# Kernel tuning notes

Measured on AMD Instinct MI355X. Metric: run time of the kernel, lower is better.

## Reference

```python
import jax, jax.numpy as jnp
import numpy as np

N_NODES = 32
N_EDGES = N_NODES * (N_NODES - 1)  # 992
BATCH = 16
SEQ = 8
BS = BATCH * SEQ  # 128 frames
D = 256  # node_latent_dim == edge_latent_dim
ITERS = 3


def gru_cell(x, h, Wih, Whh, bih, bhh):
    # torch GRUCell: gates ordered (r, z, n)
    gi = x @ Wih.T + bih
    gh = h @ Whh.T + bhh
    ir, iz, inn = jnp.split(gi, 3, axis=-1)
    hr, hz, hn = jnp.split(gh, 3, axis=-1)
    r = jax.nn.sigmoid(ir + hr)
    z = jax.nn.sigmoid(iz + hz)
    n = jnp.tanh(inn + r * hn)
    return (1.0 - z) * n + z * h


def setup_inputs() -> dict:
    key = jax.random.key(0)
    ks = jax.random.split(key, 16)
    s = 0.05
    inp = {
        'node_latents': jax.random.normal(ks[0], (BS * N_NODES, D), jnp.float32),
        'edge_latents': jax.random.normal(ks[1], (BS * N_EDGES, D), jnp.float32),
        'node_Wih': jax.random.normal(ks[2], (3 * D, D), jnp.float32) * s,
        'node_Whh': jax.random.normal(ks[3], (3 * D, D), jnp.float32) * s,
        'node_bih': jax.random.normal(ks[4], (3 * D,), jnp.float32) * s,
        'node_bhh': jax.random.normal(ks[5], (3 * D,), jnp.float32) * s,
        'edge_Wih': jax.random.normal(ks[6], (3 * D, D), jnp.float32) * s,
        'edge_Whh': jax.random.normal(ks[7], (3 * D, D), jnp.float32) * s,
        'edge_bih': jax.random.normal(ks[8], (3 * D,), jnp.float32) * s,
        'edge_bhh': jax.random.normal(ks[9], (3 * D,), jnp.float32) * s,
        'w_node_pool': jax.random.normal(ks[10], (2 * D,), jnp.float32) * s,
        'w_edge_pool_sub': jax.random.normal(ks[11], (2 * D,), jnp.float32) * s,
        'w_edge_pool_obj': jax.random.normal(ks[12], (2 * D,), jnp.float32) * s,
    }
    # all ordered (subject, object) pairs with subject != object, same for every frame
    pairs = np.array([(i, j) for i in range(N_NODES) for j in range(N_NODES) if i != j], dtype=np.int32)  # [E,2]
    e2n = np.concatenate([np.arange(N_EDGES, dtype=np.int32)[:, None], pairs], axis=1)  # [E,3]
    inp['edge_idx_to_node_idxs'] = jnp.asarray(np.broadcast_to(e2n, (BS, N_EDGES, 3)).copy())
    return inp


def reference(node_latents, edge_latents, node_Wih, node_Whh, node_bih, node_bhh,
              edge_Wih, edge_Whh, edge_bih, edge_bhh,
              w_node_pool, w_edge_pool_sub, w_edge_pool_obj, edge_idx_to_node_idxs):
    sub = edge_idx_to_node_idxs[..., 1].astype(jnp.int32)  # [BS,E]
    obj = edge_idx_to_node_idxs[..., 2].astype(jnp.int32)
    bidx = jnp.arange(BS, dtype=jnp.int32)[:, None]
    sub_flat = (bidx * N_NODES + sub).reshape(-1)  # [BS*E]
    obj_flat = (bidx * N_NODES + obj).reshape(-1)

    # initial GRU call with zero hidden state (torch GRUCell default)
    node_hidden = gru_cell(node_latents, jnp.zeros_like(node_latents), node_Wih, node_Whh, node_bih, node_bhh)
    edge_hidden = gru_cell(edge_latents, jnp.zeros_like(edge_latents), edge_Wih, edge_Whh, edge_bih, edge_bhh)

    for _ in range(ITERS):
        nh = node_hidden.reshape(BS, N_NODES, D)
        eh = edge_hidden.reshape(BS, N_EDGES, D)
        ns = jnp.take_along_axis(nh, sub[:, :, None], axis=1)  # [BS,E,D] subject node feats
        no = jnp.take_along_axis(nh, obj[:, :, None], axis=1)  # [BS,E,D]
        cat_s = jnp.concatenate([ns, eh], axis=-1)  # [BS,E,2D]
        cat_o = jnp.concatenate([no, eh], axis=-1)
        g_node = jax.nn.sigmoid(cat_s @ w_node_pool)[..., None]        # [BS,E,1]
        g_sub = jax.nn.sigmoid(cat_s @ w_edge_pool_sub)[..., None]
        g_obj = jax.nn.sigmoid(cat_o @ w_edge_pool_obj)[..., None]
        # node message: gated edge features scattered to subject and object nodes
        # (equivalent to the dense 0/1 incidence matmul since subject != object per edge)
        msg_e = (g_node * eh).reshape(-1, D)  # [BS*E,D]
        node_msg = (jax.ops.segment_sum(msg_e, sub_flat, num_segments=BS * N_NODES)
                    + jax.ops.segment_sum(msg_e, obj_flat, num_segments=BS * N_NODES))  # [BS*N,D]
        edge_msg = (g_sub * ns + g_obj * no).reshape(-1, D)  # [BS*E,D]
        node_hidden = gru_cell(node_msg, node_hidden, node_Wih, node_Whh, node_bih, node_bhh)
        edge_hidden = gru_cell(edge_msg, edge_hidden, edge_Wih, edge_Whh, edge_bih, edge_bhh)

    return (node_hidden.reshape(BS, N_NODES, D), edge_hidden.reshape(BS, N_EDGES, D))
```

## Files before the change

### kernel.cpp

```cpp
#include <hip/hip_runtime.h>


#define D_DIM 256
#define NNODE 32
#define NEDGE 992
#define EDGE_ROWS (128 * NEDGE)
#define NODE_ROWS (128 * NNODE)
#define BM 64
#define EGRID (EDGE_ROWS / BM)
#define NGRID (NODE_ROWS / BM)
#define GI_OFF 32768
#define GI_STR 776

typedef _Float16 half8 __attribute__((ext_vector_type(8)));
typedef _Float16 half4v __attribute__((ext_vector_type(4)));
typedef __attribute__((ext_vector_type(4))) float f32x4;

__device__ __forceinline__ float sigf(float x) { return 1.0f / (1.0f + __expf(-x)); }
__device__ __forceinline__ float tanh_fast(float x) { return 2.0f / (1.0f + __expf(-2.0f * x)) - 1.0f; }
__device__ __forceinline__ float dot4(float4 a, float4 b) { return a.x*b.x + a.y*b.y + a.z*b.z + a.w*b.w; }

__global__ __launch_bounds__(64) void pack_w(const float* __restrict__ Wih,
                                             const float* __restrict__ Whh,
                                             _Float16* __restrict__ ph) {
  const int ct = blockIdx.x;
  const int ks = blockIdx.y;
  const int l = threadIdx.x;
  const int col = ct * 16 + (l & 15);
  const int kb = ks * 32 + (l >> 4) * 8;
  const float* src = (kb < 256) ? (Wih + col * 256 + kb) : (Whh + col * 256 + (kb - 256));
  half8 v;
  #pragma unroll
  for (int j = 0; j < 8; ++j) v[j] = (_Float16)src[j];
  *(half8*)(ph + ((ct * 16 + ks) * 64 + l) * 8) = v;
}

__global__ __launch_bounds__(1024, 4) void gru_init(
    const float* __restrict__ xe, const float* __restrict__ xn,
    _Float16* __restrict__ eh16, float* __restrict__ hn,
    const _Float16* __restrict__ wpe, const _Float16* __restrict__ wpn,
    const float* __restrict__ ebih, const float* __restrict__ ebhh,
    const float* __restrict__ nbih, const float* __restrict__ nbhh) {
  __shared__ __align__(16) unsigned char lds[32768];
  const bool edge = blockIdx.x < EGRID;
  const int bx = edge ? blockIdx.x : (blockIdx.x - EGRID);
  const float* xsrc = edge ? xe : xn;
  const _Float16* wp = edge ? wpe : wpn;
  const float* bih = edge ? ebih : nbih;
  const float* bhh = edge ? ebhh : nbhh;

  const int t = threadIdx.x;
  const int rb = bx * BM;
  const int srow = t >> 4;
  const int skc = t & 15;
  const int w = t >> 6;
  const int l = t & 63;
  const int lq = l >> 4;
  const int lr = l & 15;
  const int swm = (lr & 7) << 4;
  const int swz = (srow & 7) << 4;
  const int rowg = rb + srow;

  #pragma unroll
  for (int c = 0; c < 2; ++c) {
    half8 hx;
    #pragma unroll
    for (int pq = 0; pq < 2; ++pq) {
      const float4 a = *(const float4*)(xsrc + rowg * D_DIM + c * 128 + skc * 8 + pq * 4);
      hx[pq * 4 + 0] = (_Float16)a.x; hx[pq * 4 + 1] = (_Float16)a.y;
      hx[pq * 4 + 2] = (_Float16)a.z; hx[pq * 4 + 3] = (_Float16)a.w;
    }
    *(half8*)(&lds[(srow * 512 + c * 256 + skc * 16) ^ swz]) = hx;
  }
  __syncthreads();

  const f32x4 zz = {0.f, 0.f, 0.f, 0.f};
  f32x4 acc_r[4] = {zz, zz, zz, zz};
  f32x4 acc_z[4] = {zz, zz, zz, zz};
  f32x4 acc_nx[4] = {zz, zz, zz, zz};

  #pragma unroll
  for (int ksg = 0; ksg < 8; ++ksg) {
    half8 ah[4];
    #pragma unroll
    for (int rf = 0; rf < 4; ++rf)
      ah[rf] = *(const half8*)(&lds[((rf * 16 + lr) * 512 + ksg * 64 + lq * 16) ^ swm]);
    const half8 br_ = *(const half8*)(wp + (((0 * 16 + w) * 16 + ksg) * 64 + l) * 8);
    const half8 bz_ = *(const half8*)(wp + (((1 * 16 + w) * 16 + ksg) * 64 + l) * 8);
    const half8 bn_ = *(const half8*)(wp + (((2 * 16 + w) * 16 + ksg) * 64 + l) * 8);
    #pragma unroll
    for (int rf = 0; rf < 4; ++rf)
      acc_r[rf] = __builtin_amdgcn_mfma_f32_16x16x32_f16(ah[rf], br_, acc_r[rf], 0, 0, 0);
    #pragma unroll
    for (int rf = 0; rf < 4; ++rf)
      acc_z[rf] = __builtin_amdgcn_mfma_f32_16x16x32_f16(ah[rf], bz_, acc_z[rf], 0, 0, 0);
    #pragma unroll
    for (int rf = 0; rf < 4; ++rf)
      acc_nx[rf] = __builtin_amdgcn_mfma_f32_16x16x32_f16(ah[rf], bn_, acc_nx[rf], 0, 0, 0);
  }

  const int col = w * 16 + lr;
  const float br = bih[col] + bhh[col];
  const float bz = bih[256 + col] + bhh[256 + col];
  const float bnx = bih[512 + col];
  const float bnh = bhh[512 + col];

  if (edge) {
    _Float16 sv[16];
    #pragma unroll
    for (int rf = 0; rf < 4; ++rf) {
      #pragma unroll
      for (int q = 0; q < 4; ++q) {
        const float r = sigf(acc_r[rf][q] + br);
        const float z = sigf(acc_z[rf][q] + bz);
        const float n = tanh_fast(acc_nx[rf][q] + bnx + r * bnh);
        sv[rf * 4 + q] = (_Float16)((1.0f - z) * n);
      }
    }
    __syncthreads();
    #pragma unroll
    for (int rf = 0; rf < 4; ++rf) {
      #pragma unroll
      for (int q = 0; q < 4; ++q) {
        const int rowl = rf * 16 + lq * 4 + q;
        *(_Float16*)(&lds[(rowl * 512 + col * 2) ^ ((rowl & 7) << 4)]) = sv[rf * 4 + q];
      }
    }
    __syncthreads();
    #pragma unroll
    for (int p = 0; p < 2; ++p) {
      const int c = t + p * 1024;
      const int row = c >> 5;
      const int kc = c & 31;
      *(uint4*)(eh16 + (rb + row) * 256 + kc * 8) =
          *(const uint4*)(&lds[(row * 512 + kc * 16) ^ ((row & 7) << 4)]);
    }
  } else {
    #pragma unroll
    for (int rf = 0; rf < 4; ++rf) {
      #pragma unroll
      for (int q = 0; q < 4; ++q) {
        const int rowl = rf * 16 + lq * 4 + q;
        const float r = sigf(acc_r[rf][q] + br);
        const float z = sigf(acc_z[rf][q] + bz);
        const float n = tanh_fast(acc_nx[rf][q] + bnx + r * bnh);
        hn[(rb + rowl) * D_DIM + col] = (1.0f - z) * n;
      }
    }
  }
}

__global__ __launch_bounds__(1024, 4) void gru_nw(
    const float* __restrict__ nh, const _Float16* __restrict__ wp,
    _Float16* __restrict__ nw,
    const float* __restrict__ wnp, const float* __restrict__ wes,
    const float* __restrict__ weo,
    float* __restrict__ dA, float* __restrict__ dS, float* __restrict__ dO) {
  __shared__ __align__(16) unsigned char lds[32768];
  const int t = threadIdx.x;
  const int rb = blockIdx.x * BM;
  const int srow = t >> 4;
  const int skc = t & 15;
  const int w = t >> 6;
  const int l = t & 63;
  const int lq = l >> 4;
  const int lr = l & 15;
  const int swm = (lr & 7) << 4;
  const int swz = (srow & 7) << 4;
  const int rowg = rb + srow;

  float4 xa[4];
  #pragma unroll
  for (int i = 0; i < 4; ++i)
    xa[i] = *(const float4*)(nh + rowg * D_DIM + (i >> 1) * 128 + skc * 8 + (i & 1) * 4);
  #pragma unroll
  for (int c = 0; c < 2; ++c) {
    half8 hx;
    const float* f0 = (const float*)&xa[c * 2];
    #pragma unroll
    for (int j = 0; j < 8; ++j) hx[j] = (_Float16)f0[j];
    *(half8*)(&lds[(srow * 512 + c * 256 + skc * 16) ^ swz]) = hx;
  }
  float p1 = 0.f, p2 = 0.f, p3 = 0.f;
  #pragma unroll
  for (int i = 0; i < 4; ++i) {
    const int k0 = (i >> 1) * 128 + skc * 8 + (i & 1) * 4;
    p1 += dot4(xa[i], *(const float4*)(wnp + k0));
    p2 += dot4(xa[i], *(const float4*)(wes + k0));
    p3 += dot4(xa[i], *(const float4*)(weo + k0));
  }
  #pragma unroll
  for (int mm = 1; mm < 16; mm <<= 1) {
    p1 += __shfl_xor(p1, mm, 16);
    p2 += __shfl_xor(p2, mm, 16);
    p3 += __shfl_xor(p3, mm, 16);
  }
  if (skc == 0) { dA[rowg] = p1; dS[rowg] = p2; dO[rowg] = p3; }
  __syncthreads();

  const f32x4 zz = {0.f, 0.f, 0.f, 0.f};
  f32x4 acc_r[4] = {zz, zz, zz, zz};
  f32x4 acc_z[4] = {zz, zz, zz, zz};
  f32x4 acc_nx[4] = {zz, zz, zz, zz};

  #pragma unroll
  for (int ksg = 0; ksg < 8; ++ksg) {
    half8 ah[4];
    #pragma unroll
    for (int rf = 0; rf < 4; ++rf)
      ah[rf] = *(const half8*)(&lds[((rf * 16 + lr) * 512 + ksg * 64 + lq * 16) ^ swm]);
    const half8 br_ = *(const half8*)(wp + (((0 * 16 + w) * 16 + ksg) * 64 + l) * 8);
    const half8 bz_ = *(const half8*)(wp + (((1 * 16 + w) * 16 + ksg) * 64 + l) * 8);
    const half8 bn_ = *(const half8*)(wp + (((2 * 16 + w) * 16 + ksg) * 64 + l) * 8);
    #pragma unroll
    for (int rf = 0; rf < 4; ++rf)
      acc_r[rf] = __builtin_amdgcn_mfma_f32_16x16x32_f16(ah[rf], br_, acc_r[rf], 0, 0, 0);
    #pragma unroll
    for (int rf = 0; rf < 4; ++rf)
      acc_z[rf] = __builtin_amdgcn_mfma_f32_16x16x32_f16(ah[rf], bz_, acc_z[rf], 0, 0, 0);
    #pragma unroll
    for (int rf = 0; rf < 4; ++rf)
      acc_nx[rf] = __builtin_amdgcn_mfma_f32_16x16x32_f16(ah[rf], bn_, acc_nx[rf], 0, 0, 0);
  }

  const int col = w * 16 + lr;
  #pragma unroll
  for (int rf = 0; rf < 4; ++rf) {
    #pragma unroll
    for (int q = 0; q < 4; ++q) {
      const int rowl = rf * 16 + lq * 4 + q;
      _Float16* np = nw + (rb + rowl) * 768 + col;
      np[0]   = (_Float16)acc_r[rf][q];
      np[256] = (_Float16)acc_z[rf][q];
      np[512] = (_Float16)acc_nx[rf][q];
    }
  }
}

template <bool LAST>
__global__ __launch_bounds__(1024, 4) void gru_iter(
    _Float16* __restrict__ eh16, float* __restrict__ ehf,
    float* __restrict__ nh, const float* __restrict__ nmsg,
    const _Float16* __restrict__ wpe, const _Float16* __restrict__ wpn,
    const float* __restrict__ ebih, const float* __restrict__ ebhh,
    const float* __restrict__ nbih, const float* __restrict__ nbhh,
    const float* __restrict__ wesb, const float* __restrict__ weob,
    const float* __restrict__ dotS, const float* __restrict__ dotO,
    const _Float16* __restrict__ nw) {
  __shared__ __align__(16) unsigned char lds[32768 + BM * GI_STR * 2];

  const int t = threadIdx.x;
  const int srow = t >> 4;
  const int skc = t & 15;
  const int w = t >> 6;
  const int l = t & 63;
  const int lq = l >> 4;
  const int lr = l & 15;
  const int swm = (lr & 7) << 4;
  const int swz = (srow & 7) << 4;

  const f32x4 zz = {0.f, 0.f, 0.f, 0.f};
  f32x4 acc_r[4] = {zz, zz, zz, zz};
  f32x4 acc_z[4] = {zz, zz, zz, zz};
  f32x4 acc_nx[4] = {zz, zz, zz, zz};
  f32x4 acc_nh[4] = {zz, zz, zz, zz};

  if (blockIdx.x < EGRID) {
    const int rb = blockIdx.x * BM;
    const int rowg = rb + srow;
    const int b = rowg / NEDGE;
    const int e = rowg - b * NEDGE;
    const int si = e / 31;
    const int m = e - si * 31;
    const int ob = (m < si) ? m : (m + 1);

    const uint4 v0 = *(const uint4*)(eh16 + rowg * 256 + skc * 8);
    const uint4 v1 = *(const uint4*)(eh16 + rowg * 256 + 128 + skc * 8);
    *(uint4*)(&lds[(srow * 512 + skc * 16) ^ swz]) = v0;
    *(uint4*)(&lds[(srow * 512 + 256 + skc * 16) ^ swz]) = v1;
    float pS = 0.f, pO = 0.f;
    {
      const _Float16* f0 = (const _Float16*)&v0;
      const _Float16* f1 = (const _Float16*)&v1;
      #pragma unroll
      for (int j = 0; j < 8; ++j) {
        const float a = (float)f0[j];
        const float bb = (float)f1[j];
        pS += a * wesb[skc * 8 + j] + bb * wesb[128 + skc * 8 + j];
        pO += a * weob[skc * 8 + j] + bb * weob[128 + skc * 8 + j];
      }
    }
    #pragma unroll
    for (int mm = 1; mm < 16; mm <<= 1) {
      pS += __shfl_xor(pS, mm, 16);
      pO += __shfl_xor(pO, mm, 16);
    }
    const float gs = sigf(dotS[b * NNODE + si] + pS);
    const float go = sigf(dotO[b * NNODE + ob] + pO);
    const _Float16 gsh = (_Float16)gs, goh = (_Float16)go;
    const _Float16* ns = nw + (b * NNODE + si) * 768;
    const _Float16* no_ = nw + (b * NNODE + ob) * 768;
    _Float16* giw = (_Float16*)(lds + GI_OFF) + srow * GI_STR;
    #pragma unroll
    for (int j = 0; j < 6; ++j) {
      const int c0 = skc * 8 + j * 128;
      const half8 a = *(const half8*)(ns + c0);
      const half8 bb = *(const half8*)(no_ + c0);
      half8 g;
      #pragma unroll
      for (int k = 0; k < 8; ++k) g[k] = gsh * a[k] + goh * bb[k];
      *(half8*)(giw + c0) = g;
    }
    __syncthreads();

    #pragma unroll
    for (int ksg = 0; ksg < 8; ++ksg) {
      half8 ah[4];
      #pragma unroll
      for (int rf = 0; rf < 4; ++rf)
        ah[rf] = *(const half8*)(&lds[((rf * 16 + lr) * 512 + ksg * 64 + lq * 16) ^ swm]);
      const int kk = 8 + ksg;
      const half8 br_ = *(const half8*)(wpe + (((0 * 16 + w) * 16 + kk) * 64 + l) * 8);
      const half8 bz_ = *(const half8*)(wpe + (((1 * 16 + w) * 16 + kk) * 64 + l) * 8);
      const half8 bn_ = *(const half8*)(wpe + (((2 * 16 + w) * 16 + kk) * 64 + l) * 8);
      #pragma unroll
      for (int rf = 0; rf < 4; ++rf)
        acc_r[rf] = __builtin_amdgcn_mfma_f32_16x16x32_f16(ah[rf], br_, acc_r[rf], 0, 0, 0);
      #pragma unroll
      for (int rf = 0; rf < 4; ++rf)
        acc_z[rf] = __builtin_amdgcn_mfma_f32_16x16x32_f16(ah[rf], bz_, acc_z[rf], 0, 0, 0);
      #pragma unroll
      for (int rf = 0; rf < 4; ++rf)
        acc_nh[rf] = __builtin_amdgcn_mfma_f32_16x16x32_f16(ah[rf], bn_, acc_nh[rf], 0, 0, 0);
    }

    const int col = w * 16 + lr;
    const float br = ebih[col] + ebhh[col];
    const float bz = ebih[256 + col] + ebhh[256 + col];
    const float bnx = ebih[512 + col];
    const float bnh = ebhh[512 + col];
    const _Float16* gir = (const _Float16*)(lds + GI_OFF);
    _Float16 sv[16];
    #pragma unroll
    for (int rf = 0; rf < 4; ++rf) {
      #pragma unroll
      for (int q = 0; q < 4; ++q) {
        const int rowl = rf * 16 + lq * 4 + q;
        const _Float16* gp = gir + rowl * GI_STR + col;
        const float r = sigf(acc_r[rf][q] + (float)gp[0] + br);
        const float z = sigf(acc_z[rf][q] + (float)gp[256] + bz);
        const float n = tanh_fast((float)gp[512] + bnx + r * (acc_nh[rf][q] + bnh));
        const float hv =
            (float)*(const _Float16*)(&lds[(rowl * 512 + col * 2) ^ ((rowl & 7) << 4)]);
        const float out = (1.0f - z) * n + z * hv;
        if constexpr (LAST) {
          ehf[(rb + rowl) * D_DIM + col] = out;
        } else {
          sv[rf * 4 + q] = (_Float16)out;
        }
      }
    }
    if constexpr (!LAST) {
      __syncthreads();
      #pragma unroll
      for (int rf = 0; rf < 4; ++rf) {
        #pragma unroll
        for (int q = 0; q < 4; ++q) {
          const int rowl = rf * 16 + lq * 4 + q;
          *(_Float16*)(&lds[(rowl * 512 + col * 2) ^ ((rowl & 7) << 4)]) = sv[rf * 4 + q];
        }
      }
      __syncthreads();
      #pragma unroll
      for (int p = 0; p < 2; ++p) {
        const int c = t + p * 1024;
        const int row = c >> 5;
        const int kc = c & 31;
        *(uint4*)(eh16 + (rb + row) * 256 + kc * 8) =
            *(const uint4*)(&lds[(row * 512 + kc * 16) ^ ((row & 7) << 4)]);
      }
    }
  } else {
    const int rb = (blockIdx.x - EGRID) * BM;
    const int rowg = rb + srow;

    {
      float4 pre[4];
      #pragma unroll
      for (int i = 0; i < 4; ++i)
        pre[i] = *(const float4*)(nh + rowg * D_DIM + (i >> 1) * 128 + skc * 8 + (i & 1) * 4);
      #pragma unroll
      for (int c = 0; c < 2; ++c) {
        half8 hh8;
        const float* f1 = (const float*)&pre[c * 2];
        #pragma unroll
        for (int j = 0; j < 8; ++j) hh8[j] = (_Float16)f1[j];
        *(half8*)(&lds[(srow * 1024 + 512 + c * 256 + skc * 16) ^ swz]) = hh8;
      }
    }
    __syncthreads();

    #pragma unroll
    for (int ksg = 0; ksg < 8; ++ksg) {
      half8 ah[4];
      #pragma unroll
      for (int rf = 0; rf < 4; ++rf)
        ah[rf] = *(const half8*)(&lds[((rf * 16 + lr) * 1024 + 512 + ksg * 64 + lq * 16) ^ swm]);
      const int kk = 8 + ksg;
      const half8 br_ = *(const half8*)(wpn + (((0 * 16 + w) * 16 + kk) * 64 + l) * 8);
      const half8 bz_ = *(const half8*)(wpn + (((1 * 16 + w) * 16 + kk) * 64 + l) * 8);
      const half8 bn_ = *(const half8*)(wpn + (((2 * 16 + w) * 16 + kk) * 64 + l) * 8);
      #pragma unroll
      for (int rf = 0; rf < 4; ++rf)
        acc_r[rf] = __builtin_amdgcn_mfma_f32_16x16x32_f16(ah[rf], br_, acc_r[rf], 0, 0, 0);
      #pragma unroll
      for (int rf = 0; rf < 4; ++rf)
        acc_z[rf] = __builtin_amdgcn_mfma_f32_16x16x32_f16(ah[rf], bz_, acc_z[rf], 0, 0, 0);
      #pragma unroll
      for (int rf = 0; rf < 4; ++rf)
        acc_nh[rf] = __builtin_amdgcn_mfma_f32_16x16x32_f16(ah[rf], bn_, acc_nh[rf], 0, 0, 0);
    }

    #pragma unroll
    for (int c = 0; c < 2; ++c) {
      half8 hx;
      #pragma unroll
      for (int pq = 0; pq < 2; ++pq) {
        const float4 a = *(const float4*)(nmsg + rowg * D_DIM + c * 128 + skc * 8 + pq * 4);
        hx[pq * 4 + 0] = (_Float16)a.x; hx[pq * 4 + 1] = (_Float16)a.y;
        hx[pq * 4 + 2] = (_Float16)a.z; hx[pq * 4 + 3] = (_Float16)a.w;
      }
      *(half8*)(&lds[(srow * 1024 + 0 + c * 256 + skc * 16) ^ swz]) = hx;
    }
    __syncthreads();
    #pragma unroll
    for (int ksg = 0; ksg < 8; ++ksg) {
      half8 ah[4];
      #pragma unroll
      for (int rf = 0; rf < 4; ++rf)
        ah[rf] = *(const half8*)(&lds[((rf * 16 + lr) * 1024 + 0 + ksg * 64 + lq * 16) ^ swm]);
      const half8 br_ = *(const half8*)(wpn + (((0 * 16 + w) * 16 + ksg) * 64 + l) * 8);
      const half8 bz_ = *(const half8*)(wpn + (((1 * 16 + w) * 16 + ksg) * 64 + l) * 8);
      const half8 bn_ = *(const half8*)(wpn + (((2 * 16 + w) * 16 + ksg) * 64 + l) * 8);
      #pragma unroll
      for (int rf = 0; rf < 4; ++rf)
        acc_r[rf] = __builtin_amdgcn_mfma_f32_16x16x32_f16(ah[rf], br_, acc_r[rf], 0, 0, 0);
      #pragma unroll
      for (int rf = 0; rf < 4; ++rf)
        acc_z[rf] = __builtin_amdgcn_mfma_f32_16x16x32_f16(ah[rf], bz_, acc_z[rf], 0, 0, 0);
      #pragma unroll
      for (int rf = 0; rf < 4; ++rf)
        acc_nx[rf] = __builtin_amdgcn_mfma_f32_16x16x32_f16(ah[rf], bn_, acc_nx[rf], 0, 0, 0);
    }

    const int col = w * 16 + lr;
    const float br = nbih[col] + nbhh[col];
    const float bz = nbih[256 + col] + nbhh[256 + col];
    const float bnx = nbih[512 + col];
    const float bnh = nbhh[512 + col];
    #pragma unroll
    for (int rf = 0; rf < 4; ++rf) {
      #pragma unroll
      for (int q = 0; q < 4; ++q) {
        const int rowl = rf * 16 + lq * 4 + q;
        const float r = sigf(acc_r[rf][q] + br);
        const float z = sigf(acc_z[rf][q] + bz);
        const float n = tanh_fast(acc_nx[rf][q] + bnx + r * (acc_nh[rf][q] + bnh));
        const float hv = nh[(rb + rowl) * D_DIM + col];
        nh[(rb + rowl) * D_DIM + col] = (1.0f - z) * n + z * hv;
      }
    }
  }
}

__global__ __launch_bounds__(256) void node_msg_kernel(
    const _Float16* __restrict__ eh16, const float* __restrict__ wnp,
    const float* __restrict__ dotA, float* __restrict__ nmsg) {
  __shared__ float sh[3][256];
  const int nr = blockIdx.x;
  const int b = nr >> 5;
  const int n = nr & 31;
  const int wv = threadIdx.x >> 6;
  const int l = threadIdx.x & 63;
  const int base = b * NEDGE;
  const float4 w1b = ((const float4*)(wnp + 256))[l];

  float4 acc = {0.f, 0.f, 0.f, 0.f};
  for (int k = wv; k < 62; k += 4) {
    int e, sub;
    if (k < 31) {
      e = base + n * 31 + k;
      sub = n;
    } else {
      int i = k - 31;
      const int ip = (i < n) ? i : (i + 1);
      e = base + ip * 31 + ((n < ip) ? n : (n - 1));
      sub = ip;
    }
    const half4v hv4 = ((const half4v*)(eh16 + e * 256))[l];
    float4 ev;
    ev.x = (float)hv4[0]; ev.y = (float)hv4[1];
    ev.z = (float)hv4[2]; ev.w = (float)hv4[3];
    float p = dot4(ev, w1b);
    #pragma unroll
    for (int mm = 32; mm > 0; mm >>= 1) p += __shfl_xor(p, mm, 64);
    const float gN = sigf(dotA[b * NNODE + sub] + p);
    acc.x += gN * ev.x; acc.y += gN * ev.y; acc.z += gN * ev.z; acc.w += gN * ev.w;
  }
  if (wv > 0) *(float4*)(&sh[wv - 1][l * 4]) = acc;
  __syncthreads();
  if (wv == 0) {
    #pragma unroll
    for (int v = 0; v < 3; ++v) {
      const float4 o = *(const float4*)(&sh[v][l * 4]);
      acc.x += o.x; acc.y += o.y; acc.z += o.z; acc.w += o.w;
    }
    *(float4*)(nmsg + nr * D_DIM + l * 4) = acc;
  }
}

extern "C" void kernel_launch(void* const* d_in, const int* in_sizes, int n_in,
                              void* d_out, int out_size, void* d_ws, size_t ws_size,
                              hipStream_t stream) {
  const float* node_latents = (const float*)d_in[0];
  const float* edge_latents = (const float*)d_in[1];
  const float* node_Wih = (const float*)d_in[2];
  const float* node_Whh = (const float*)d_in[3];
  const float* node_bih = (const float*)d_in[4];
  const float* node_bhh = (const float*)d_in[5];
  const float* edge_Wih = (const float*)d_in[6];
  const float* edge_Whh = (const float*)d_in[7];
  const float* edge_bih = (const float*)d_in[8];
  const float* edge_bhh = (const float*)d_in[9];
  const float* w_node_pool = (const float*)d_in[10];
  const float* w_edge_sub = (const float*)d_in[11];
  const float* w_edge_obj = (const float*)d_in[12];

  float* nh = (float*)d_out;
  float* eh = (float*)d_out + NODE_ROWS * D_DIM;

  const int WPLANE = 48 * 16 * 64 * 8;
  _Float16* ph_n = (_Float16*)d_ws;
  _Float16* ph_e = ph_n + WPLANE;
  _Float16* NW = ph_e + WPLANE;
  _Float16* eh16 = NW + NODE_ROWS * 768;
  float* fw = (float*)(eh16 + (size_t)EDGE_ROWS * D_DIM);
  float* dotA = fw; fw += NODE_ROWS;
  float* dotS = fw; fw += NODE_ROWS;
  float* dotO = fw; fw += NODE_ROWS;
  float* node_msg = fw; fw += NODE_ROWS * D_DIM;

  dim3 pg(48, 16);
  pack_w<<<pg, 64, 0, stream>>>(node_Wih, node_Whh, ph_n);
  pack_w<<<pg, 64, 0, stream>>>(edge_Wih, edge_Whh, ph_e);

  gru_init<<<EGRID + NGRID, 1024, 0, stream>>>(
      edge_latents, node_latents, eh16, nh, ph_e, ph_n,
      edge_bih, edge_bhh, node_bih, node_bhh);

  for (int it = 0; it < 3; ++it) {
    gru_nw<<<NGRID, 1024, 0, stream>>>(
        nh, ph_e, NW, w_node_pool, w_edge_sub, w_edge_obj, dotA, dotS, dotO);
    node_msg_kernel<<<NODE_ROWS, 256, 0, stream>>>(eh16, w_node_pool, dotA, node_msg);
    if (it < 2)
      gru_iter<false><<<EGRID + NGRID, 1024, 0, stream>>>(
          eh16, eh, nh, node_msg, ph_e, ph_n,
          edge_bih, edge_bhh, node_bih, node_bhh,
          w_edge_sub + 256, w_edge_obj + 256, dotS, dotO, NW);
    else
      gru_iter<true><<<EGRID + NGRID, 1024, 0, stream>>>(
          eh16, eh, nh, node_msg, ph_e, ph_n,
          edge_bih, edge_bhh, node_bih, node_bhh,
          w_edge_sub + 256, w_edge_obj + 256, dotS, dotO, NW);
  }
}
```

Measured before the change: 656.4 us.

## Fuse node-message kernel into node GEMM launch and double-buffer init tiles

Merges the node-message gather/reduction into the same launch as the node hidden projection. Extra blocks compute the node-pool dot products locally in LDS instead of reading them from a global buffer written by the earlier kernel. That removes one launch and one global round trip per iteration. The init kernel now processes two 64-row tiles per block, prefetching the second tile's input while the first tile computes, using a 64KB LDS double buffer. The larger LDS footprint may reduce occupancy, and it halves the init grid.

```diff
diff --git a/kernel.cpp b/kernel.cpp
--- a/kernel.cpp
+++ b/kernel.cpp
@@ -41,16 +41,15 @@
     const _Float16* __restrict__ wpe, const _Float16* __restrict__ wpn,
     const float* __restrict__ ebih, const float* __restrict__ ebhh,
     const float* __restrict__ nbih, const float* __restrict__ nbhh) {
-  __shared__ __align__(16) unsigned char lds[32768];
-  const bool edge = blockIdx.x < EGRID;
-  const int bx = edge ? blockIdx.x : (blockIdx.x - EGRID);
+  __shared__ __align__(16) unsigned char lds[65536];
+  const bool edge = blockIdx.x < (EGRID / 2);
   const float* xsrc = edge ? xe : xn;
   const _Float16* wp = edge ? wpe : wpn;
   const float* bih = edge ? ebih : nbih;
   const float* bhh = edge ? ebhh : nbhh;
+  const int tb = edge ? (blockIdx.x * 2) : ((blockIdx.x - EGRID / 2) * 2);
 
   const int t = threadIdx.x;
-  const int rb = bx * BM;
   const int srow = t >> 4;
   const int skc = t & 15;
   const int w = t >> 6;
@@ -59,45 +58,6 @@
   const int lr = l & 15;
   const int swm = (lr & 7) << 4;
   const int swz = (srow & 7) << 4;
-  const int rowg = rb + srow;
-
-  #pragma unroll
-  for (int c = 0; c < 2; ++c) {
-    half8 hx;
-    #pragma unroll
-    for (int pq = 0; pq < 2; ++pq) {
-      const float4 a = *(const float4*)(xsrc + rowg * D_DIM + c * 128 + skc * 8 + pq * 4);
-      hx[pq * 4 + 0] = (_Float16)a.x; hx[pq * 4 + 1] = (_Float16)a.y;
-      hx[pq * 4 + 2] = (_Float16)a.z; hx[pq * 4 + 3] = (_Float16)a.w;
-    }
-    *(half8*)(&lds[(srow * 512 + c * 256 + skc * 16) ^ swz]) = hx;
-  }
-  __syncthreads();
-
-  const f32x4 zz = {0.f, 0.f, 0.f, 0.f};
-  f32x4 acc_r[4] = {zz, zz, zz, zz};
-  f32x4 acc_z[4] = {zz, zz, zz, zz};
-  f32x4 acc_nx[4] = {zz, zz, zz, zz};
-
-  #pragma unroll
-  for (int ksg = 0; ksg < 8; ++ksg) {
-    half8 ah[4];
-    #pragma unroll
-    for (int rf = 0; rf < 4; ++rf)
-      ah[rf] = *(const half8*)(&lds[((rf * 16 + lr) * 512 + ksg * 64 + lq * 16) ^ swm]);
-    const half8 br_ = *(const half8*)(wp + (((0 * 16 + w) * 16 + ksg) * 64 + l) * 8);
-    const half8 bz_ = *(const half8*)(wp + (((1 * 16 + w) * 16 + ksg) * 64 + l) * 8);
-    const half8 bn_ = *(const half8*)(wp + (((2 * 16 + w) * 16 + ksg) * 64 + l) * 8);
-    #pragma unroll
-    for (int rf = 0; rf < 4; ++rf)
-      acc_r[rf] = __builtin_amdgcn_mfma_f32_16x16x32_f16(ah[rf], br_, acc_r[rf], 0, 0, 0);
-    #pragma unroll
-    for (int rf = 0; rf < 4; ++rf)
-      acc_z[rf] = __builtin_amdgcn_mfma_f32_16x16x32_f16(ah[rf], bz_, acc_z[rf], 0, 0, 0);
-    #pragma unroll
-    for (int rf = 0; rf < 4; ++rf)
-      acc_nx[rf] = __builtin_amdgcn_mfma_f32_16x16x32_f16(ah[rf], bn_, acc_nx[rf], 0, 0, 0);
-  }
 
   const int col = w * 16 + lr;
   const float br = bih[col] + bhh[col];
@@ -105,134 +65,249 @@
   const float bnx = bih[512 + col];
   const float bnh = bhh[512 + col];
 
-  if (edge) {
-    _Float16 sv[16];
-    #pragma unroll
-    for (int rf = 0; rf < 4; ++rf) {
-      #pragma unroll
-      for (int q = 0; q < 4; ++q) {
-        const float r = sigf(acc_r[rf][q] + br);
-        const float z = sigf(acc_z[rf][q] + bz);
-        const float n = tanh_fast(acc_nx[rf][q] + bnx + r * bnh);
-        sv[rf * 4 + q] = (_Float16)((1.0f - z) * n);
-      }
-    }
-    __syncthreads();
-    #pragma unroll
-    for (int rf = 0; rf < 4; ++rf) {
-      #pragma unroll
-      for (int q = 0; q < 4; ++q) {
-        const int rowl = rf * 16 + lq * 4 + q;
-        *(_Float16*)(&lds[(rowl * 512 + col * 2) ^ ((rowl & 7) << 4)]) = sv[rf * 4 + q];
-      }
-    }
-    __syncthreads();
-    #pragma unroll
-    for (int p = 0; p < 2; ++p) {
-      const int c = t + p * 1024;
-      const int row = c >> 5;
-      const int kc = c & 31;
-      *(uint4*)(eh16 + (rb + row) * 256 + kc * 8) =
-          *(const uint4*)(&lds[(row * 512 + kc * 16) ^ ((row & 7) << 4)]);
-    }
-  } else {
-    #pragma unroll
-    for (int rf = 0; rf < 4; ++rf) {
-      #pragma unroll
-      for (int q = 0; q < 4; ++q) {
-        const int rowl = rf * 16 + lq * 4 + q;
-        const float r = sigf(acc_r[rf][q] + br);
-        const float z = sigf(acc_z[rf][q] + bz);
-        const float n = tanh_fast(acc_nx[rf][q] + bnx + r * bnh);
-        hn[(rb + rowl) * D_DIM + col] = (1.0f - z) * n;
-      }
-    }
-  }
+  float4 xa[4];
+  auto LOAD = [&](int tile) {
+    const int rowg = tile * BM + srow;
+    #pragma unroll
+    for (int i = 0; i < 4; ++i)
+      xa[i] = *(const float4*)(xsrc + rowg * D_DIM + (i >> 1) * 128 + skc * 8 + (i & 1) * 4);
+  };
+  auto STAGE = [&](int buf) {
+    #pragma unroll
+    for (int c = 0; c < 2; ++c) {
+      half8 hx;
+      const float* f0 = (const float*)&xa[c * 2];
+      #pragma unroll
+      for (int j = 0; j < 8; ++j) hx[j] = (_Float16)f0[j];
+      *(half8*)(&lds[buf * 32768 + ((srow * 512 + c * 256 + skc * 16) ^ swz)]) = hx;
+    }
+  };
+
+  f32x4 acc_r[4], acc_z[4], acc_nx[4];
+  auto COMPUTE = [&](int buf) {
+    const f32x4 zz = {0.f, 0.f, 0.f, 0.f};
+    #pragma unroll
+    for (int rf = 0; rf < 4; ++rf) { acc_r[rf] = zz; acc_z[rf] = zz; acc_nx[rf] = zz; }
+    #pragma unroll
+    for (int ksg = 0; ksg < 8; ++ksg) {
+      half8 ah[4];
+      #pragma unroll
+      for (int rf = 0; rf < 4; ++rf)
+        ah[rf] = *(const half8*)(&lds[buf * 32768 + (((rf * 16 + lr) * 512 + ksg * 64 + lq * 16) ^ swm)]);
+      const half8 br_ = *(const half8*)(wp + (((0 * 16 + w) * 16 + ksg) * 64 + l) * 8);
+      const half8 bz_ = *(const half8*)(wp + (((1 * 16 + w) * 16 + ksg) * 64 + l) * 8);
+      const half8 bn_ = *(const half8*)(wp + (((2 * 16 + w) * 16 + ksg) * 64 + l) * 8);
+      #pragma unroll
+      for (int rf = 0; rf < 4; ++rf)
+        acc_r[rf] = __builtin_amdgcn_mfma_f32_16x16x32_f16(ah[rf], br_, acc_r[rf], 0, 0, 0);
+      #pragma unroll
+      for (int rf = 0; rf < 4; ++rf)
+        acc_z[rf] = __builtin_amdgcn_mfma_f32_16x16x32_f16(ah[rf], bz_, acc_z[rf], 0, 0, 0);
+      #pragma unroll
+      for (int rf = 0; rf < 4; ++rf)
+        acc_nx[rf] = __builtin_amdgcn_mfma_f32_16x16x32_f16(ah[rf], bn_, acc_nx[rf], 0, 0, 0);
+    }
+  };
+
+  auto EPILOGUE = [&](int tile, int buf) {
+    const int rb = tile * BM;
+    if (edge) {
+      _Float16 sv[16];
+      #pragma unroll
+      for (int rf = 0; rf < 4; ++rf) {
+        #pragma unroll
+        for (int q = 0; q < 4; ++q) {
+          const float r = sigf(acc_r[rf][q] + br);
+          const float z = sigf(acc_z[rf][q] + bz);
+          const float n = tanh_fast(acc_nx[rf][q] + bnx + r * bnh);
+          sv[rf * 4 + q] = (_Float16)((1.0f - z) * n);
+        }
+      }
+      __syncthreads();
+      #pragma unroll
+      for (int rf = 0; rf < 4; ++rf) {
+        #pragma unroll
+        for (int q = 0; q < 4; ++q) {
+          const int rowl = rf * 16 + lq * 4 + q;
+          *(_Float16*)(&lds[buf * 32768 + ((rowl * 512 + col * 2) ^ ((rowl & 7) << 4))]) = sv[rf * 4 + q];
+        }
+      }
+      __syncthreads();
+      #pragma unroll
+      for (int p = 0; p < 2; ++p) {
+        const int c = t + p * 1024;
+        const int row = c >> 5;
+        const int kc = c & 31;
+        *(uint4*)(eh16 + (rb + row) * 256 + kc * 8) =
+            *(const uint4*)(&lds[buf * 32768 + ((row * 512 + kc * 16) ^ ((row & 7) << 4))]);
+      }
+    } else {
+      #pragma unroll
+      for (int rf = 0; rf < 4; ++rf) {
+        #pragma unroll
+        for (int q = 0; q < 4; ++q) {
+          const int rowl = rf * 16 + lq * 4 + q;
+          const float r = sigf(acc_r[rf][q] + br);
+          const float z = sigf(acc_z[rf][q] + bz);
+          const float n = tanh_fast(acc_nx[rf][q] + bnx + r * bnh);
+          hn[(rb + rowl) * D_DIM + col] = (1.0f - z) * n;
+        }
+      }
+    }
+  };
+
+  LOAD(tb); STAGE(0); __syncthreads();
+  LOAD(tb + 1);
+  COMPUTE(0);
+  EPILOGUE(tb, 0);
+  STAGE(1); __syncthreads();
+  COMPUTE(1);
+  EPILOGUE(tb + 1, 1);
 }
 
-__global__ __launch_bounds__(1024, 4) void gru_nw(
+__global__ __launch_bounds__(1024, 4) void gru_nw_msg(
     const float* __restrict__ nh, const _Float16* __restrict__ wp,
     _Float16* __restrict__ nw,
     const float* __restrict__ wnp, const float* __restrict__ wes,
     const float* __restrict__ weo,
-    float* __restrict__ dA, float* __restrict__ dS, float* __restrict__ dO) {
+    float* __restrict__ dS, float* __restrict__ dO,
+    const _Float16* __restrict__ eh16, float* __restrict__ nmsg) {
   __shared__ __align__(16) unsigned char lds[32768];
   const int t = threadIdx.x;
-  const int rb = blockIdx.x * BM;
-  const int srow = t >> 4;
-  const int skc = t & 15;
-  const int w = t >> 6;
-  const int l = t & 63;
-  const int lq = l >> 4;
-  const int lr = l & 15;
-  const int swm = (lr & 7) << 4;
-  const int swz = (srow & 7) << 4;
-  const int rowg = rb + srow;
-
-  float4 xa[4];
-  #pragma unroll
-  for (int i = 0; i < 4; ++i)
-    xa[i] = *(const float4*)(nh + rowg * D_DIM + (i >> 1) * 128 + skc * 8 + (i & 1) * 4);
-  #pragma unroll
-  for (int c = 0; c < 2; ++c) {
-    half8 hx;
-    const float* f0 = (const float*)&xa[c * 2];
-    #pragma unroll
-    for (int j = 0; j < 8; ++j) hx[j] = (_Float16)f0[j];
-    *(half8*)(&lds[(srow * 512 + c * 256 + skc * 16) ^ swz]) = hx;
-  }
-  float p1 = 0.f, p2 = 0.f, p3 = 0.f;
-  #pragma unroll
-  for (int i = 0; i < 4; ++i) {
-    const int k0 = (i >> 1) * 128 + skc * 8 + (i & 1) * 4;
-    p1 += dot4(xa[i], *(const float4*)(wnp + k0));
-    p2 += dot4(xa[i], *(const float4*)(wes + k0));
-    p3 += dot4(xa[i], *(const float4*)(weo + k0));
-  }
-  #pragma unroll
-  for (int mm = 1; mm < 16; mm <<= 1) {
-    p1 += __shfl_xor(p1, mm, 16);
-    p2 += __shfl_xor(p2, mm, 16);
-    p3 += __shfl_xor(p3, mm, 16);
-  }
-  if (skc == 0) { dA[rowg] = p1; dS[rowg] = p2; dO[rowg] = p3; }
-  __syncthreads();
-
-  const f32x4 zz = {0.f, 0.f, 0.f, 0.f};
-  f32x4 acc_r[4] = {zz, zz, zz, zz};
-  f32x4 acc_z[4] = {zz, zz, zz, zz};
-  f32x4 acc_nx[4] = {zz, zz, zz, zz};
-
-  #pragma unroll
-  for (int ksg = 0; ksg < 8; ++ksg) {
-    half8 ah[4];
-    #pragma unroll
-    for (int rf = 0; rf < 4; ++rf)
-      ah[rf] = *(const half8*)(&lds[((rf * 16 + lr) * 512 + ksg * 64 + lq * 16) ^ swm]);
-    const half8 br_ = *(const half8*)(wp + (((0 * 16 + w) * 16 + ksg) * 64 + l) * 8);
-    const half8 bz_ = *(const half8*)(wp + (((1 * 16 + w) * 16 + ksg) * 64 + l) * 8);
-    const half8 bn_ = *(const half8*)(wp + (((2 * 16 + w) * 16 + ksg) * 64 + l) * 8);
-    #pragma unroll
-    for (int rf = 0; rf < 4; ++rf)
-      acc_r[rf] = __builtin_amdgcn_mfma_f32_16x16x32_f16(ah[rf], br_, acc_r[rf], 0, 0, 0);
-    #pragma unroll
-    for (int rf = 0; rf < 4; ++rf)
-      acc_z[rf] = __builtin_amdgcn_mfma_f32_16x16x32_f16(ah[rf], bz_, acc_z[rf], 0, 0, 0);
-    #pragma unroll
-    for (int rf = 0; rf < 4; ++rf)
-      acc_nx[rf] = __builtin_amdgcn_mfma_f32_16x16x32_f16(ah[rf], bn_, acc_nx[rf], 0, 0, 0);
-  }
-
-  const int col = w * 16 + lr;
-  #pragma unroll
-  for (int rf = 0; rf < 4; ++rf) {
-    #pragma unroll
-    for (int q = 0; q < 4; ++q) {
-      const int rowl = rf * 16 + lq * 4 + q;
-      _Float16* np = nw + (rb + rowl) * 768 + col;
-      np[0]   = (_Float16)acc_r[rf][q];
-      np[256] = (_Float16)acc_z[rf][q];
-      np[512] = (_Float16)acc_nx[rf][q];
+
+  if (blockIdx.x < NGRID) {
+    const int rb = blockIdx.x * BM;
+    const int srow = t >> 4;
+    const int skc = t & 15;
+    const int w = t >> 6;
+    const int l = t & 63;
+    const int lq = l >> 4;
+    const int lr = l & 15;
+    const int swm = (lr & 7) << 4;
+    const int swz = (srow & 7) << 4;
+    const int rowg = rb + srow;
+
+    float4 xa[4];
+    #pragma unroll
+    for (int i = 0; i < 4; ++i)
+      xa[i] = *(const float4*)(nh + rowg * D_DIM + (i >> 1) * 128 + skc * 8 + (i & 1) * 4);
+    #pragma unroll
+    for (int c = 0; c < 2; ++c) {
+      half8 hx;
+      const float* f0 = (const float*)&xa[c * 2];
+      #pragma unroll
+      for (int j = 0; j < 8; ++j) hx[j] = (_Float16)f0[j];
+      *(half8*)(&lds[(srow * 512 + c * 256 + skc * 16) ^ swz]) = hx;
+    }
+    float p2 = 0.f, p3 = 0.f;
+    #pragma unroll
+    for (int i = 0; i < 4; ++i) {
+      const int k0 = (i >> 1) * 128 + skc * 8 + (i & 1) * 4;
+      p2 += dot4(xa[i], *(const float4*)(wes + k0));
+      p3 += dot4(xa[i], *(const float4*)(weo + k0));
+    }
+    #pragma unroll
+    for (int mm = 1; mm < 16; mm <<= 1) {
+      p2 += __shfl_xor(p2, mm, 16);
+      p3 += __shfl_xor(p3, mm, 16);
+    }
+    if (skc == 0) { dS[rowg] = p2; dO[rowg] = p3; }
+    __syncthreads();
+
+    const f32x4 zz = {0.f, 0.f, 0.f, 0.f};
+    f32x4 acc_r[4] = {zz, zz, zz, zz};
+    f32x4 acc_z[4] = {zz, zz, zz, zz};
+    f32x4 acc_nx[4] = {zz, zz, zz, zz};
+
+    #pragma unroll
+    for (int ksg = 0; ksg < 8; ++ksg) {
+      half8 ah[4];
+      #pragma unroll
+      for (int rf = 0; rf < 4; ++rf)
+        ah[rf] = *(const half8*)(&lds[((rf * 16 + lr) * 512 + ksg * 64 + lq * 16) ^ swm]);
+      const half8 br_ = *(const half8*)(wp + (((0 * 16 + w) * 16 + ksg) * 64 + l) * 8);
+      const half8 bz_ = *(const half8*)(wp + (((1 * 16 + w) * 16 + ksg) * 64 + l) * 8);
+      const half8 bn_ = *(const half8*)(wp + (((2 * 16 + w) * 16 + ksg) * 64 + l) * 8);
+      #pragma unroll
+      for (int rf = 0; rf < 4; ++rf)
+        acc_r[rf] = __builtin_amdgcn_mfma_f32_16x16x32_f16(ah[rf], br_, acc_r[rf], 0, 0, 0);
+      #pragma unroll
+      for (int rf = 0; rf < 4; ++rf)
+        acc_z[rf] = __builtin_amdgcn_mfma_f32_16x16x32_f16(ah[rf], bz_, acc_z[rf], 0, 0, 0);
+      #pragma unroll
+      for (int rf = 0; rf < 4; ++rf)
+        acc_nx[rf] = __builtin_amdgcn_mfma_f32_16x16x32_f16(ah[rf], bn_, acc_nx[rf], 0, 0, 0);
+    }
+
+    const int col = w * 16 + lr;
+    #pragma unroll
+    for (int rf = 0; rf < 4; ++rf) {
+      #pragma unroll
+      for (int q = 0; q < 4; ++q) {
+        const int rowl = rf * 16 + lq * 4 + q;
+        _Float16* np = nw + (rb + rowl) * 768 + col;
+        np[0]   = (_Float16)acc_r[rf][q];
+        np[256] = (_Float16)acc_z[rf][q];
+        np[512] = (_Float16)acc_nx[rf][q];
+      }
+    }
+  } else {
+    float (*sh)[3][256] = (float (*)[3][256])lds;
+    float* dotA_s = (float*)(lds + 12288);
+    const int nb = blockIdx.x - NGRID;
+    const int b = nb >> 3;
+    const int wg = t >> 6;
+    const int l = t & 63;
+    const int base = b * NEDGE;
+    const float4 w1a = ((const float4*)wnp)[l];
+    const float4 w1b = ((const float4*)(wnp + 256))[l];
+
+    #pragma unroll
+    for (int u = 0; u < 2; ++u) {
+      const int nn = wg * 2 + u;
+      float p = dot4(((const float4*)(nh + (b * NNODE + nn) * D_DIM))[l], w1a);
+      #pragma unroll
+      for (int mm = 32; mm > 0; mm >>= 1) p += __shfl_xor(p, mm, 64);
+      if (l == 0) dotA_s[nn] = p;
+    }
+    __syncthreads();
+
+    const int node_local = wg >> 2;
+    const int wv = wg & 3;
+    const int n = (nb & 7) * 4 + node_local;
+    const int nr = b * NNODE + n;
+
+    float4 acc = {0.f, 0.f, 0.f, 0.f};
+    for (int k = wv; k < 62; k += 4) {
+      int e, sub;
+      if (k < 31) {
+        e = base + n * 31 + k;
+        sub = n;
+      } else {
+        int i = k - 31;
+        const int ip = (i < n) ? i : (i + 1);
+        e = base + ip * 31 + ((n < ip) ? n : (n - 1));
+        sub = ip;
+      }
+      const half4v hv4 = ((const half4v*)(eh16 + e * 256))[l];
+      float4 ev;
+      ev.x = (float)hv4[0]; ev.y = (float)hv4[1];
+      ev.z = (float)hv4[2]; ev.w = (float)hv4[3];
+      float p = dot4(ev, w1b);
+      #pragma unroll
+      for (int mm = 32; mm > 0; mm >>= 1) p += __shfl_xor(p, mm, 64);
+      const float gN = sigf(dotA_s[sub] + p);
+      acc.x += gN * ev.x; acc.y += gN * ev.y; acc.z += gN * ev.z; acc.w += gN * ev.w;
+    }
+    if (wv > 0) *(float4*)(&sh[node_local][wv - 1][l * 4]) = acc;
+    __syncthreads();
+    if (wv == 0) {
+      #pragma unroll
+      for (int v = 0; v < 3; ++v) {
+        const float4 o = *(const float4*)(&sh[node_local][v][l * 4]);
+        acc.x += o.x; acc.y += o.y; acc.z += o.z; acc.w += o.w;
+      }
+      *(float4*)(nmsg + nr * D_DIM + l * 4) = acc;
     }
   }
 }
@@ -470,52 +545,6 @@
         nh[(rb + rowl) * D_DIM + col] = (1.0f - z) * n + z * hv;
       }
     }
-  }
-}
-
-__global__ __launch_bounds__(256) void node_msg_kernel(
-    const _Float16* __restrict__ eh16, const float* __restrict__ wnp,
-    const float* __restrict__ dotA, float* __restrict__ nmsg) {
-  __shared__ float sh[3][256];
-  const int nr = blockIdx.x;
-  const int b = nr >> 5;
-  const int n = nr & 31;
-  const int wv = threadIdx.x >> 6;
-  const int l = threadIdx.x & 63;
-  const int base = b * NEDGE;
-  const float4 w1b = ((const float4*)(wnp + 256))[l];
-
-  float4 acc = {0.f, 0.f, 0.f, 0.f};
-  for (int k = wv; k < 62; k += 4) {
-    int e, sub;
-    if (k < 31) {
-      e = base + n * 31 + k;
-      sub = n;
-    } else {
-      int i = k - 31;
-      const int ip = (i < n) ? i : (i + 1);
-      e = base + ip * 31 + ((n < ip) ? n : (n - 1));
-      sub = ip;
-    }
-    const half4v hv4 = ((const half4v*)(eh16 + e * 256))[l];
-    float4 ev;
-    ev.x = (float)hv4[0]; ev.y = (float)hv4[1];
-    ev.z = (float)hv4[2]; ev.w = (float)hv4[3];
-    float p = dot4(ev, w1b);
-    #pragma unroll
-    for (int mm = 32; mm > 0; mm >>= 1) p += __shfl_xor(p, mm, 64);
-    const float gN = sigf(dotA[b * NNODE + sub] + p);
-    acc.x += gN * ev.x; acc.y += gN * ev.y; acc.z += gN * ev.z; acc.w += gN * ev.w;
-  }
-  if (wv > 0) *(float4*)(&sh[wv - 1][l * 4]) = acc;
-  __syncthreads();
-  if (wv == 0) {
-    #pragma unroll
-    for (int v = 0; v < 3; ++v) {
-      const float4 o = *(const float4*)(&sh[v][l * 4]);
-      acc.x += o.x; acc.y += o.y; acc.z += o.z; acc.w += o.w;
-    }
-    *(float4*)(nmsg + nr * D_DIM + l * 4) = acc;
   }
 }
 
@@ -545,7 +574,6 @@
   _Float16* NW = ph_e + WPLANE;
   _Float16* eh16 = NW + NODE_ROWS * 768;
   float* fw = (float*)(eh16 + (size_t)EDGE_ROWS * D_DIM);
-  float* dotA = fw; fw += NODE_ROWS;
   float* dotS = fw; fw += NODE_ROWS;
   float* dotO = fw; fw += NODE_ROWS;
   float* node_msg = fw; fw += NODE_ROWS * D_DIM;
@@ -554,14 +582,14 @@
   pack_w<<<pg, 64, 0, stream>>>(node_Wih, node_Whh, ph_n);
   pack_w<<<pg, 64, 0, stream>>>(edge_Wih, edge_Whh, ph_e);
 
-  gru_init<<<EGRID + NGRID, 1024, 0, stream>>>(
+  gru_init<<<(EGRID + NGRID) / 2, 1024, 0, stream>>>(
       edge_latents, node_latents, eh16, nh, ph_e, ph_n,
       edge_bih, edge_bhh, node_bih, node_bhh);
 
   for (int it = 0; it < 3; ++it) {
-    gru_nw<<<NGRID, 1024, 0, stream>>>(
-        nh, ph_e, NW, w_node_pool, w_edge_sub, w_edge_obj, dotA, dotS, dotO);
-    node_msg_kernel<<<NODE_ROWS, 256, 0, stream>>>(eh16, w_node_pool, dotA, node_msg);
+    gru_nw_msg<<<NGRID + 1024, 1024, 0, stream>>>(
+        nh, ph_e, NW, w_node_pool, w_edge_sub, w_edge_obj,
+        dotS, dotO, eh16, node_msg);
     if (it < 2)
       gru_iter<false><<<EGRID + NGRID, 1024, 0, stream>>>(
           eh16, eh, nh, node_msg, ph_e, ph_n,
```

Measured after the change: 715.8 us. 1.09x slower.
